# Kernel optimization log

Measured on AMD Instinct MI355X. Metric: run time of the kernel, lower is better.

The kernel has to match this reference:

```python
import jax, jax.numpy as jnp
import numpy as np

N = 120000   # nodes
E = 1200000  # edges
F_IN = 14    # PascalVOC-SP node features
H = 64       # args.hidden
C = 21       # num_classes
EPS = 1e-5


def _glorot(k, shape):
    fan_in = shape[0]
    return jax.random.normal(k, shape, jnp.float32) / np.sqrt(fan_in).astype(np.float32)


def setup_inputs() -> dict:
    key = jax.random.key(0)
    ks = jax.random.split(key, 16)
    inp = {}
    inp['x1'] = jax.random.normal(ks[0], (N, F_IN), jnp.float32)
    inp['edge_index'] = jax.random.randint(ks[1], (2, E), 0, N)
    dims = [(F_IN, H), (H, H), (H, H), (H, H)]
    i = 2
    for l, (din, dout) in enumerate(dims, 1):
        inp[f'Wn{l}'] = _glorot(ks[i], (din, dout)); i += 1
        inp[f'Wr{l}'] = _glorot(ks[i], (din, dout)); i += 1
        inp[f'b{l}'] = jnp.zeros((dout,), jnp.float32)
    for l in (1, 2, 3):
        inp[f'g{l}'] = jnp.ones((H,), jnp.float32)
        inp[f'be{l}'] = jnp.zeros((H,), jnp.float32)
    inp['Wm0'] = _glorot(ks[10], (H, H))
    inp['gm0'] = jnp.ones((H,), jnp.float32)
    inp['bem0'] = jnp.zeros((H,), jnp.float32)
    inp['Wm1'] = _glorot(ks[11], (H, H))
    inp['gm1'] = jnp.ones((H,), jnp.float32)
    inp['bem1'] = jnp.zeros((H,), jnp.float32)
    inp['Wm2'] = _glorot(ks[12], (H, C))
    inp['bm2'] = jnp.zeros((C,), jnp.float32)
    return inp


def _bn(x, g, b):
    # BatchNorm1d forward with batch statistics (train-mode normalization, biased var)
    m = x.mean(axis=0)
    v = x.var(axis=0)
    return (x - m) * jax.lax.rsqrt(v + EPS) * g + b


def _sage(x, src, dst, Wn, Wr, b):
    # PyG SAGEConv (mean aggr): out = mean_neighbors @ Wn + b + x @ Wr
    s = jax.ops.segment_sum(x[src], dst, num_segments=N)        # [N, d]
    cnt = jax.ops.segment_sum(jnp.ones((src.shape[0],), x.dtype), dst, num_segments=N)
    mean = s / jnp.maximum(cnt, 1.0)[:, None]
    return mean @ Wn + b + x @ Wr


def _lrelu(z):
    return jnp.where(z > 0, z, 0.01 * z)


def reference(x1, edge_index, Wn1, Wr1, b1, Wn2, Wr2, b2, Wn3, Wr3, b3, Wn4, Wr4, b4,
              g1, be1, g2, be2, g3, be3, Wm0, gm0, bem0, Wm1, gm1, bem1, Wm2, bm2):
    src, dst = edge_index[0], edge_index[1]
    x = _bn(_lrelu(_sage(x1, src, dst, Wn1, Wr1, b1)), g1, be1)   # conv1 + bano1 (dropout off)
    x = _bn(_lrelu(_sage(x, src, dst, Wn2, Wr2, b2)), g2, be2)    # conv2 + bano2
    x = _bn(jax.nn.relu(_sage(x, src, dst, Wn3, Wr3, b3)), g3, be3)  # conv3 + bano3
    x = _sage(x, src, dst, Wn4, Wr4, b4)                          # conv4
    # mlpRep: Linear(no bias)->BN->ReLU x2, then Linear(bias), no final act
    x = jax.nn.relu(_bn(x @ Wm0, gm0, bem0))
    x = jax.nn.relu(_bn(x @ Wm1, gm1, bem1))
    return x @ Wm2 + bm2
```

## Files before the change

kernel.cpp:

```cpp
#include <hip/hip_runtime.h>

constexpr int NN = 120000;
constexpr int EE = 1200000;
constexpr float EPSV = 1e-5f;
constexpr int NCBLK   = (NN + 127) / 128;
constexpr int NMFMABLK = NN / 64;
constexpr int ASTRIDE = 32;
constexpr int NSLOT = 64;

constexpr int BNODES  = 128;
constexpr int NBUCK   = (NN + BNODES - 1) / BNODES;
constexpr int BSTRIDE = 1536;
constexpr int EPB3    = 4096;
constexpr int NB3     = (EE + EPB3 - 1) / EPB3;
constexpr int NSTATF  = 5*NSLOT*128;

typedef __attribute__((ext_vector_type(8))) short bf8v;
typedef __attribute__((ext_vector_type(4))) float f4v;

__device__ __forceinline__ float bf2f(unsigned short u){
  union { unsigned i; float f; } v; v.i = ((unsigned)u) << 16; return v.f;
}
__device__ __forceinline__ unsigned short f2bf(float f){
  union { float f; unsigned i; } v; v.f = f;
  unsigned u = v.i;
  return (unsigned short)((u + 0x7FFFu + ((u >> 16) & 1u)) >> 16);
}
__device__ __forceinline__ unsigned pack2(float a, float b){
  return (unsigned)f2bf(a) | ((unsigned)f2bf(b) << 16);
}
__device__ __forceinline__ float act_f(float z, int ACT){
  if (ACT == 1) return z > 0.0f ? z : 0.01f*z;
  if (ACT == 2) return fmaxf(z, 0.0f);
  return z;
}
__device__ __forceinline__ void acc8(uint4 u, float& a0, float& a1, float& a2, float& a3,
                                     float& a4, float& a5, float& a6, float& a7){
  a0 += bf2f((unsigned short)(u.x & 0xFFFF)); a1 += bf2f((unsigned short)(u.x >> 16));
  a2 += bf2f((unsigned short)(u.y & 0xFFFF)); a3 += bf2f((unsigned short)(u.y >> 16));
  a4 += bf2f((unsigned short)(u.z & 0xFFFF)); a5 += bf2f((unsigned short)(u.z >> 16));
  a6 += bf2f((unsigned short)(u.w & 0xFFFF)); a7 += bf2f((unsigned short)(u.w >> 16));
}

__global__ __launch_bounds__(512) void k_bucket(const int* __restrict__ src, const int* __restrict__ dst,
                                                int* __restrict__ cursor, unsigned* __restrict__ bucketed,
                                                float* __restrict__ stats,
                                                const float* __restrict__ x, unsigned* __restrict__ xb){
  __shared__ int hist[NBUCK];
  __shared__ int lstart[NBUCK];
  const int tid = threadIdx.x;
  const int e0  = blockIdx.x * EPB3;
  for (int i = blockIdx.x*512 + tid; i < NSTATF; i += NB3*512) stats[i] = 0.0f;
  for (int i = blockIdx.x*512 + tid; i < NN*8; i += NB3*512){
    int n = i >> 3, j = i & 7;
    int c0 = 2*j, c1 = 2*j + 1;
    float f0 = (c0 < 14) ? x[(size_t)n*14 + c0] : 0.0f;
    float f1 = (c1 < 14) ? x[(size_t)n*14 + c1] : 0.0f;
    xb[i] = pack2(f0, f1);
  }
  for (int i = tid; i < NBUCK; i += 512) hist[i] = 0;
  __syncthreads();

  const bool full = (e0 + EPB3 <= EE);
  if (full){
    #pragma unroll 4
    for (int k = 0; k < EPB3/512; k++){
      int d = dst[e0 + k*512 + tid];
      atomicAdd(&hist[d >> 7], 1);
    }
  } else {
    #pragma unroll 1
    for (int k = 0; k < EPB3/512; k++){
      int e = e0 + k*512 + tid;
      if (e < EE){
        int d = dst[e];
        atomicAdd(&hist[d >> 7], 1);
      }
    }
  }
  __syncthreads();
  for (int i = tid; i < NBUCK; i += 512){
    int h = hist[i];
    lstart[i] = (h > 0) ? atomicAdd(&cursor[i], h) : 0;
  }
  __syncthreads();
  for (int i = tid; i < NBUCK; i += 512) hist[i] = 0;
  __syncthreads();
  #pragma unroll 1
  for (int k = 0; k < EPB3/512; k++){
    int e = e0 + k*512 + tid;
    if (e < EE){
      int d = dst[e];
      int s = src[e];
      int b = d >> 7;
      int r = atomicAdd(&hist[b], 1);
      int idx = lstart[b] + r;
      if (idx < BSTRIDE)
        bucketed[(size_t)b*BSTRIDE + idx] = ((unsigned)s << 7) | (unsigned)(d & 127);
    }
  }
}

__global__ __launch_bounds__(256) void k_buildadj(const unsigned* __restrict__ bucketed,
                                                  const int* __restrict__ cursor,
                                                  int* __restrict__ cnt, int* __restrict__ adj,
                                                  float* __restrict__ invdeg){
  __shared__ alignas(16) int ladj[BNODES*ASTRIDE];
  __shared__ int lcnt[BNODES];
  const int tid = threadIdx.x;
  const int b   = blockIdx.x;
  if (tid < BNODES) lcnt[tid] = 0;
  __syncthreads();
  const int tot = min(cursor[b], BSTRIDE);
  const unsigned* rp = bucketed + (size_t)b*BSTRIDE;
  for (int e = tid; e < tot; e += 256){
    unsigned rec = rp[e];
    int d = (int)(rec & 127u);
    int s = (int)(rec >> 7);
    int p = atomicAdd(&lcnt[d], 1);
    if (p < ASTRIDE) ladj[d*ASTRIDE + p] = s;
  }
  __syncthreads();
  int4* ap = (int4*)(adj + (size_t)b*BNODES*ASTRIDE);
  const int4* lp = (const int4*)ladj;
  #pragma unroll
  for (int i = 0; i < (BNODES*ASTRIDE/4)/256; i++)
    ap[i*256 + tid] = lp[i*256 + tid];
  if (tid < BNODES){
    int c = lcnt[tid];
    int n = b*BNODES + tid;
    cnt[n] = c;
    invdeg[n] = (c > 0) ? (1.0f/(float)c) : -1.0f;
  }
}

__global__ __launch_bounds__(256) void k_prep_conv_frag(const float* __restrict__ Wn, const float* __restrict__ Wr,
                                                        const float* __restrict__ b, const float* __restrict__ statSlots,
                                                        const float* __restrict__ g, const float* __restrict__ be,
                                                        unsigned short* __restrict__ frag, float* __restrict__ bias2){
  __shared__ float sc[64], sh[64];
  int t = threadIdx.x;
  if (t < 64){
    float sum = 0.0f, sq = 0.0f;
    #pragma unroll 8
    for (int s = 0; s < NSLOT; s++){
      sum += statSlots[s*128 + t];
      sq  += statSlots[s*128 + 64 + t];
    }
    float m = sum * (1.0f/NN);
    float v = sq * (1.0f/NN) - m*m;
    float a = g[t] * rsqrtf(v + EPSV);
    sc[t] = a; sh[t] = be[t] - m*a;
  }
  __syncthreads();
  if (blockIdx.x == 0 && t < 64){
    float accB = b[t], accN = 0.0f;
    for (int k=0;k<64;k++){
      accB += sh[k]*Wr[k*64+t];
      accN += sh[k]*Wn[k*64+t];
    }
    bias2[t]      = accB;
    bias2[64 + t] = accN;
  }
  {
    int idx = blockIdx.x*256 + t;
    int j    = idx & 7;
    int lane = (idx >> 3) & 63;
    int kk   = (idx >> 9) & 1;
    int ct   = (idx >> 10) & 3;
    int mat  = (idx >> 12) & 1;
    int k    = kk*32 + (lane >> 4)*8 + j;
    int col  = ct*16 + (lane & 15);
    const float* W = mat ? Wr : Wn;
    frag[idx] = f2bf(sc[k] * W[k*64 + col]);
  }
}

__global__ __launch_bounds__(256) void k_prep_lin_frag(const float* __restrict__ W,
                                                       unsigned short* __restrict__ frag,
                                                       float* __restrict__ bias2,
                                                       const float* __restrict__ bnSlots,
                                                       float* __restrict__ bnRed){
  int t = threadIdx.x;
  if (blockIdx.x == 0 && t < 128){
    bias2[t] = 0.0f;
    if (bnSlots){
      float s = 0.0f;
      #pragma unroll 8
      for (int sl = 0; sl < NSLOT; sl++) s += bnSlots[sl*128 + t];
      bnRed[t] = s;
    }
  }
  {
    int idx = blockIdx.x*256 + t;
    int j    = idx & 7;
    int lane = (idx >> 3) & 63;
    int kk   = (idx >> 9) & 1;
    int ct   = (idx >> 10) & 3;
    int k    = kk*32 + (lane >> 4)*8 + j;
    int col  = ct*16 + (lane & 15);
    frag[idx] = f2bf(W[k*64 + col]);
  }
}

__global__ __launch_bounds__(64) void k_prep_aff(const float* __restrict__ st,
                                                 const float* __restrict__ g, const float* __restrict__ be,
                                                 float* __restrict__ aff){
  int t = threadIdx.x;
  float s = 0.0f, q = 0.0f;
  #pragma unroll 8
  for (int sl = 0; sl < NSLOT; sl++){
    s += st[sl*128 + t];
    q += st[sl*128 + 64 + t];
  }
  float m = s*(1.0f/NN);
  float v = q*(1.0f/NN) - m*m;
  float a = g[t]*rsqrtf(v+EPSV);
  aff[t]      = a;
  aff[64 + t] = be[t] - m*a;
}

template<int ACT, bool STATS>
__global__ __launch_bounds__(256, 1) void k_gmfma(const unsigned short* __restrict__ X,
                                                  const int* __restrict__ cnt, const int* __restrict__ adj,
                                                  const float* __restrict__ invdeg,
                                                  const unsigned short* __restrict__ frag,
                                                  const float* __restrict__ bias2,
                                                  unsigned short* __restrict__ out,
                                                  float* __restrict__ statsOut){
  __shared__ unsigned short sMean[64*72];
  __shared__ float sst[512];
  const int tid  = threadIdx.x;
  const int lane = tid & 63;
  const int wv   = tid >> 6;
  const int nb0  = blockIdx.x*64;

  {
    const int q8 = lane & 7;
    const int h8 = lane >> 3;
    #pragma unroll
    for (int t8 = 0; t8 < 2; t8++){
      const int row = wv*16 + h8*2 + t8;
      const int n   = nb0 + row;
      const int d   = min(cnt[n], ASTRIDE);
      const int st  = n*ASTRIDE;
      float a0=0,a1=0,a2=0,a3=0,a4=0,a5=0,a6=0,a7=0;
      int j = 0;
      for (; j + 7 < d; j += 8){
        int4 sa = *(const int4*)(adj + st + j);
        int4 sb = *(const int4*)(adj + st + j + 4);
        uint4 u0 = *(const uint4*)(X + (size_t)sa.x*64 + 8*q8);
        uint4 u1 = *(const uint4*)(X + (size_t)sa.y*64 + 8*q8);
        uint4 u2 = *(const uint4*)(X + (size_t)sa.z*64 + 8*q8);
        uint4 u3 = *(const uint4*)(X + (size_t)sa.w*64 + 8*q8);
        uint4 u4 = *(const uint4*)(X + (size_t)sb.x*64 + 8*q8);
        uint4 u5 = *(const uint4*)(X + (size_t)sb.y*64 + 8*q8);
        uint4 u6 = *(const uint4*)(X + (size_t)sb.z*64 + 8*q8);
        uint4 u7 = *(const uint4*)(X + (size_t)sb.w*64 + 8*q8);
        acc8(u0,a0,a1,a2,a3,a4,a5,a6,a7); acc8(u1,a0,a1,a2,a3,a4,a5,a6,a7);
        acc8(u2,a0,a1,a2,a3,a4,a5,a6,a7); acc8(u3,a0,a1,a2,a3,a4,a5,a6,a7);
        acc8(u4,a0,a1,a2,a3,a4,a5,a6,a7); acc8(u5,a0,a1,a2,a3,a4,a5,a6,a7);
        acc8(u6,a0,a1,a2,a3,a4,a5,a6,a7); acc8(u7,a0,a1,a2,a3,a4,a5,a6,a7);
      }
      for (; j + 3 < d; j += 4){
        int4 sa = *(const int4*)(adj + st + j);
        uint4 u0 = *(const uint4*)(X + (size_t)sa.x*64 + 8*q8);
        uint4 u1 = *(const uint4*)(X + (size_t)sa.y*64 + 8*q8);
        uint4 u2 = *(const uint4*)(X + (size_t)sa.z*64 + 8*q8);
        uint4 u3 = *(const uint4*)(X + (size_t)sa.w*64 + 8*q8);
        acc8(u0,a0,a1,a2,a3,a4,a5,a6,a7); acc8(u1,a0,a1,a2,a3,a4,a5,a6,a7);
        acc8(u2,a0,a1,a2,a3,a4,a5,a6,a7); acc8(u3,a0,a1,a2,a3,a4,a5,a6,a7);
      }
      for (; j < d; j++){
        int s = adj[st + j];
        uint4 u = *(const uint4*)(X + (size_t)s*64 + 8*q8);
        acc8(u,a0,a1,a2,a3,a4,a5,a6,a7);
      }
      float iv = fmaxf(invdeg[n], 0.0f);
      uint4 o;
      o.x = pack2(a0*iv, a1*iv);
      o.y = pack2(a2*iv, a3*iv);
      o.z = pack2(a4*iv, a5*iv);
      o.w = pack2(a6*iv, a7*iv);
      *(uint4*)(sMean + row*72 + 8*q8) = o;
    }
  }

  const bf8v* fp = (const bf8v*)frag;
  bf8v wn[4][2], wr[4][2];
  #pragma unroll
  for (int ct=0;ct<4;ct++){
    #pragma unroll
    for (int kk=0;kk<2;kk++){
      wn[ct][kk] = fp[((0*4+ct)*2+kk)*64 + lane];
      wr[ct][kk] = fp[((1*4+ct)*2+kk)*64 + lane];
    }
  }
  const int m  = lane & 15;
  const int kq = lane >> 4;
  const size_t arow = (size_t)(nb0 + wv*16 + m)*64;
  bf8v ax0 = *(const bf8v*)(X + arow + kq*8);
  bf8v ax1 = *(const bf8v*)(X + arow + 32 + kq*8);
  __syncthreads();
  bf8v am0 = *(const bf8v*)(sMean + (wv*16 + m)*72 + kq*8);
  bf8v am1 = *(const bf8v*)(sMean + (wv*16 + m)*72 + 32 + kq*8);

  f4v acc[4];
  #pragma unroll
  for (int ct=0;ct<4;ct++){
    f4v c = {0.0f,0.0f,0.0f,0.0f};
    c = __builtin_amdgcn_mfma_f32_16x16x32_bf16(am0, wn[ct][0], c, 0,0,0);
    c = __builtin_amdgcn_mfma_f32_16x16x32_bf16(am1, wn[ct][1], c, 0,0,0);
    c = __builtin_amdgcn_mfma_f32_16x16x32_bf16(ax0, wr[ct][0], c, 0,0,0);
    c = __builtin_amdgcn_mfma_f32_16x16x32_bf16(ax1, wr[ct][1], c, 0,0,0);
    acc[ct] = c;
  }

  const int col = lane & 15;
  float bb[4], bg[4];
  #pragma unroll
  for (int ct=0;ct<4;ct++){
    bb[ct] = bias2[ct*16 + col];
    bg[ct] = bias2[64 + ct*16 + col];
  }
  float ls[4] = {0,0,0,0}, lq[4] = {0,0,0,0};
  #pragma unroll
  for (int r=0;r<4;r++){
    const int node = nb0 + wv*16 + (lane>>4)*4 + r;
    float gadd = (invdeg[node] > 0.0f) ? 1.0f : 0.0f;
    #pragma unroll
    for (int ct=0;ct<4;ct++){
      float z = acc[ct][r] + bb[ct] + gadd * bg[ct];
      z = act_f(z, ACT);
      out[(size_t)node*64 + ct*16 + col] = f2bf(z);
      if (STATS){ ls[ct] += z; lq[ct] = fmaf(z, z, lq[ct]); }
    }
  }
  if constexpr (STATS){
    #pragma unroll
    for (int ct=0;ct<4;ct++){
      float s = ls[ct]; s += __shfl_down(s, 32); s += __shfl_down(s, 16);
      float q = lq[ct]; q += __shfl_down(q, 32); q += __shfl_down(q, 16);
      if (kq == 0){
        sst[wv*128 + ct*16 + col]      = s;
        sst[wv*128 + 64 + ct*16 + col] = q;
      }
    }
    __syncthreads();
    if (tid < 128){
      float v = sst[tid] + sst[128+tid] + sst[256+tid] + sst[384+tid];
      atomicAdd(&statsOut[(blockIdx.x & (NSLOT-1))*128 + tid], v);
    }
  }
}

template<int ACT, bool STATS, bool BNA>
__global__ __launch_bounds__(256, 1) void k_mfma_lin(const unsigned short* __restrict__ Ax,
                                                     const unsigned short* __restrict__ frag,
                                                     const float* __restrict__ bias2,
                                                     unsigned short* __restrict__ out,
                                                     float* __restrict__ statsOut,
                                                     const float* __restrict__ bnRed,
                                                     const float* __restrict__ bnG,
                                                     const float* __restrict__ bnB){
  __shared__ float sst[512];
  const int lane = threadIdx.x & 63;
  const int wv   = threadIdx.x >> 6;
  const int n0   = (blockIdx.x*4 + wv)*16;
  const int m    = lane & 15;
  const int kq   = lane >> 4;

  const bf8v* fp = (const bf8v*)frag;
  bf8v wr[4][2];
  #pragma unroll
  for (int ct=0;ct<4;ct++){
    #pragma unroll
    for (int kk=0;kk<2;kk++) wr[ct][kk] = fp[(ct*2+kk)*64 + lane];
  }

  const size_t arow = (size_t)(n0 + m)*64;
  bf8v ax0 = *(const bf8v*)(Ax + arow + kq*8);
  bf8v ax1 = *(const bf8v*)(Ax + arow + 32 + kq*8);
  if constexpr (BNA){
    #pragma unroll
    for (int j=0;j<8;j++){
      int k0 = kq*8 + j, k1 = 32 + kq*8 + j;
      float m0 = bnRed[k0]*(1.0f/NN);
      float v0 = bnRed[64+k0]*(1.0f/NN) - m0*m0;
      float a0 = bnG[k0]*rsqrtf(v0+EPSV);
      float b0 = bnB[k0] - m0*a0;
      ax0[j] = (short)f2bf(fmaxf(fmaf(a0, bf2f((unsigned short)ax0[j]), b0), 0.0f));
      float m1 = bnRed[k1]*(1.0f/NN);
      float v1 = bnRed[64+k1]*(1.0f/NN) - m1*m1;
      float a1 = bnG[k1]*rsqrtf(v1+EPSV);
      float b1 = bnB[k1] - m1*a1;
      ax1[j] = (short)f2bf(fmaxf(fmaf(a1, bf2f((unsigned short)ax1[j]), b1), 0.0f));
    }
  }

  f4v acc[4];
  #pragma unroll
  for (int ct=0;ct<4;ct++){
    f4v c = {0.0f,0.0f,0.0f,0.0f};
    c = __builtin_amdgcn_mfma_f32_16x16x32_bf16(ax0, wr[ct][0], c, 0,0,0);
    c = __builtin_amdgcn_mfma_f32_16x16x32_bf16(ax1, wr[ct][1], c, 0,0,0);
    acc[ct] = c;
  }

  const int col = lane & 15;
  float bb[4];
  #pragma unroll
  for (int ct=0;ct<4;ct++) bb[ct] = bias2[ct*16 + col];
  float ls[4] = {0,0,0,0}, lq[4] = {0,0,0,0};
  #pragma unroll
  for (int r=0;r<4;r++){
    const int node = n0 + (lane>>4)*4 + r;
    #pragma unroll
    for (int ct=0;ct<4;ct++){
      float z = act_f(acc[ct][r] + bb[ct], ACT);
      out[(size_t)node*64 + ct*16 + col] = f2bf(z);
      if (STATS){ ls[ct] += z; lq[ct] = fmaf(z, z, lq[ct]); }
    }
  }
  if constexpr (STATS){
    #pragma unroll
    for (int ct=0;ct<4;ct++){
      float s = ls[ct]; s += __shfl_down(s, 32); s += __shfl_down(s, 16);
      float q = lq[ct]; q += __shfl_down(q, 32); q += __shfl_down(q, 16);
      if (kq == 0){
        sst[wv*128 + ct*16 + col]      = s;
        sst[wv*128 + 64 + ct*16 + col] = q;
      }
    }
    __syncthreads();
    if (threadIdx.x < 128){
      float v = sst[threadIdx.x] + sst[128+threadIdx.x] + sst[256+threadIdx.x] + sst[384+threadIdx.x];
      atomicAdd(&statsOut[(blockIdx.x & (NSLOT-1))*128 + threadIdx.x], v);
    }
  }
}

__global__ __launch_bounds__(512, 1) void k_conv1(const unsigned* __restrict__ xb, const float* __restrict__ x,
                                                  const int* __restrict__ cnt, const int* __restrict__ adj,
                                                  const float* __restrict__ invdeg,
                                                  const float* __restrict__ Wn, const float* __restrict__ Wr,
                                                  const float* __restrict__ b,
                                                  unsigned short* __restrict__ out, float* __restrict__ statsOut){
  constexpr int DIN = 14, RS = 15;
  __shared__ float sMean[128*RS];
  __shared__ float sX[128*RS];
  __shared__ float sst[8*128];
  const int tid  = threadIdx.x;
  const int lane = tid & 63;
  const int wv   = tid >> 6;
  const int p    = tid & 3;
  const int nl   = tid >> 2;
  const int n0   = blockIdx.x*128;
  const int n    = n0 + nl;
  const bool valid = (n < NN);
  const int c0   = p*16;

  {
    const float* gp = x + (size_t)n0*DIN;
    for (int i = tid; i < 128*DIN; i += 512){
      int r = i / DIN, c = i - r*DIN;
      sX[r*RS + c] = (n0 + r < NN) ? gp[i] : 0.0f;
    }
  }

  {
    float mm[14];
    #pragma unroll
    for (int j=0;j<14;j++) mm[j] = 0.0f;
    const int d  = valid ? min(cnt[n], ASTRIDE) : 0;
    const int st = n*ASTRIDE;
    for (int j=p; j<d; j+=4){
      int s = adj[st+j];
      const uint4* rp = (const uint4*)(xb + s*8);
      uint4 u0 = rp[0], u1 = rp[1];
      mm[0]+=bf2f((unsigned short)(u0.x&0xFFFF)); mm[1]+=bf2f((unsigned short)(u0.x>>16));
      mm[2]+=bf2f((unsigned short)(u0.y&0xFFFF)); mm[3]+=bf2f((unsigned short)(u0.y>>16));
      mm[4]+=bf2f((unsigned short)(u0.z&0xFFFF)); mm[5]+=bf2f((unsigned short)(u0.z>>16));
      mm[6]+=bf2f((unsigned short)(u0.w&0xFFFF)); mm[7]+=bf2f((unsigned short)(u0.w>>16));
      mm[8]+=bf2f((unsigned short)(u1.x&0xFFFF)); mm[9]+=bf2f((unsigned short)(u1.x>>16));
      mm[10]+=bf2f((unsigned short)(u1.y&0xFFFF)); mm[11]+=bf2f((unsigned short)(u1.y>>16));
      mm[12]+=bf2f((unsigned short)(u1.z&0xFFFF)); mm[13]+=bf2f((unsigned short)(u1.z>>16));
    }
    #pragma unroll
    for (int j=0;j<14;j++){
      mm[j] += __shfl_xor(mm[j], 1);
      mm[j] += __shfl_xor(mm[j], 2);
    }
    float iv = valid ? invdeg[n] : -1.0f;
    float gate = (iv > 0.0f) ? iv : 0.0f;
    if (p == 0){
      #pragma unroll
      for (int j=0;j<14;j++) sMean[nl*RS + j] = mm[j]*gate;
    }
  }
  __syncthreads();

  float acc[16];
  #pragma unroll
  for (int jj=0;jj<16;jj++) acc[jj] = 0.0f;
  #pragma unroll 1
  for (int k=0;k<DIN;k++){
    float rv = sMean[nl*RS + k];
    const float* wr = Wn + k*64 + c0;
    #pragma unroll
    for (int jj=0;jj<16;jj++) acc[jj] = fmaf(wr[jj], rv, acc[jj]);
  }
  #pragma unroll 1
  for (int k=0;k<DIN;k++){
    float rv = sX[nl*RS + k];
    const float* wr = Wr + k*64 + c0;
    #pragma unroll
    for (int jj=0;jj<16;jj++) acc[jj] = fmaf(wr[jj], rv, acc[jj]);
  }

  float vs[16], vq[16];
  #pragma unroll
  for (int q=0;q<16;q++){
    float z = valid ? act_f(acc[q] + b[c0+q], 1) : 0.0f;
    vs[q] = z; vq[q] = z*z;
  }
  if (valid){
    uint4 t0, t1;
    t0.x = pack2(vs[0],vs[1]);   t0.y = pack2(vs[2],vs[3]);
    t0.z = pack2(vs[4],vs[5]);   t0.w = pack2(vs[6],vs[7]);
    t1.x = pack2(vs[8],vs[9]);   t1.y = pack2(vs[10],vs[11]);
    t1.z = pack2(vs[12],vs[13]); t1.w = pack2(vs[14],vs[15]);
    uint4* op = (uint4*)(out + (size_t)n*64 + c0);
    op[0] = t0; op[1] = t1;
  }

  #pragma unroll
  for (int k=0;k<4;k++){
    const bool keep1 = ((lane >> (k+2)) & 1) != 0;
    const int half = 16 >> (k+1);
    #pragma unroll
    for (int i=0;i<half;i++){
      float sa = vs[2*i], sb = vs[2*i+1];
      float qa = vq[2*i], qb = vq[2*i+1];
      float skeep = keep1 ? sb : sa;
      float ssend = keep1 ? sa : sb;
      float qkeep = keep1 ? qb : qa;
      float qsend = keep1 ? qa : qb;
      vs[i] = skeep + __shfl_xor(ssend, 4<<k);
      vq[i] = qkeep + __shfl_xor(qsend, 4<<k);
    }
  }
  const int f = c0 + (lane>>2);
  sst[wv*128 + f]      = vs[0];
  sst[wv*128 + 64 + f] = vq[0];
  __syncthreads();
  if (tid < 128){
    float v = 0.0f;
    #pragma unroll
    for (int w=0;w<8;w++) v += sst[w*128 + tid];
    atomicAdd(&statsOut[(blockIdx.x & (NSLOT-1))*128 + tid], v);
  }
}

__global__ __launch_bounds__(256, 1) void k_lin21(const unsigned short* __restrict__ x,
                                                  const float* __restrict__ W, const float* __restrict__ bias,
                                                  const float* __restrict__ aff,
                                                  float* __restrict__ out){
  __shared__ float sW[64*21];
  __shared__ float sAff[128];
  const int tid = threadIdx.x;
  if (tid < 128) sAff[tid] = aff[tid];
  for (int i = tid; i < 64*21; i += 256) sW[i] = W[i];
  __syncthreads();

  const int p  = tid & 3;
  const int nl = tid >> 2;
  const int n  = blockIdx.x*64 + nl;
  const bool valid = (n < NN);
  const int k0 = p*16;

  uint4 u0 = {0,0,0,0}, u1 = {0,0,0,0};
  if (valid){
    const unsigned short* rp = x + (size_t)n*64 + k0;
    u0 = *(const uint4*)(rp);
    u1 = *(const uint4*)(rp + 8);
  }
  float f[16];
  f[0]=bf2f((unsigned short)(u0.x&0xFFFF)); f[1]=bf2f((unsigned short)(u0.x>>16));
  f[2]=bf2f((unsigned short)(u0.y&0xFFFF)); f[3]=bf2f((unsigned short)(u0.y>>16));
  f[4]=bf2f((unsigned short)(u0.z&0xFFFF)); f[5]=bf2f((unsigned short)(u0.z>>16));
  f[6]=bf2f((unsigned short)(u0.w&0xFFFF)); f[7]=bf2f((unsigned short)(u0.w>>16));
  f[8]=bf2f((unsigned short)(u1.x&0xFFFF)); f[9]=bf2f((unsigned short)(u1.x>>16));
  f[10]=bf2f((unsigned short)(u1.y&0xFFFF)); f[11]=bf2f((unsigned short)(u1.y>>16));
  f[12]=bf2f((unsigned short)(u1.z&0xFFFF)); f[13]=bf2f((unsigned short)(u1.z>>16));
  f[14]=bf2f((unsigned short)(u1.w&0xFFFF)); f[15]=bf2f((unsigned short)(u1.w>>16));
  #pragma unroll
  for (int j=0;j<16;j++)
    f[j] = fmaxf(fmaf(sAff[k0+j], f[j], sAff[64+k0+j]), 0.0f);

  float a[21];
  #pragma unroll
  for (int jj=0;jj<21;jj++) a[jj] = 0.0f;
  #pragma unroll
  for (int k=0;k<16;k++){
    const float* wr = sW + (k0+k)*21;
    float rv = f[k];
    #pragma unroll
    for (int jj=0;jj<21;jj++) a[jj] = fmaf(wr[jj], rv, a[jj]);
  }
  #pragma unroll
  for (int jj=0;jj<21;jj++){
    a[jj] += __shfl_xor(a[jj], 1);
    a[jj] += __shfl_xor(a[jj], 2);
  }
  if (valid){
    const int c0 = p*6;
    const int ce = (p == 3) ? 21 : c0 + 6;
    float* op = out + (size_t)n*21;
    #pragma unroll 6
    for (int jj=c0; jj<ce; jj++) op[jj] = a[jj] + bias[jj];
  }
}

extern "C" void kernel_launch(void* const* d_in, const int* in_sizes, int n_in,
                              void* d_out, int out_size, void* d_ws, size_t ws_size,
                              hipStream_t stream){
  const float* x1  = (const float*)d_in[0];
  const int*   ei  = (const int*)d_in[1];
  const int* srcp = ei;
  const int* dstp = ei + EE;
  const float *Wn1=(const float*)d_in[2],  *Wr1=(const float*)d_in[3],  *b1=(const float*)d_in[4];
  const float *Wn2=(const float*)d_in[5],  *Wr2=(const float*)d_in[6],  *b2=(const float*)d_in[7];
  const float *Wn3=(const float*)d_in[8],  *Wr3=(const float*)d_in[9],  *b3=(const float*)d_in[10];
  const float *Wn4=(const float*)d_in[11], *Wr4=(const float*)d_in[12], *b4=(const float*)d_in[13];
  const float *g1=(const float*)d_in[14], *be1=(const float*)d_in[15];
  const float *g2=(const float*)d_in[16], *be2=(const float*)d_in[17];
  const float *g3=(const float*)d_in[18], *be3=(const float*)d_in[19];
  const float *Wm0=(const float*)d_in[20], *gm0=(const float*)d_in[21], *bem0=(const float*)d_in[22];
  const float *Wm1=(const float*)d_in[23], *gm1=(const float*)d_in[24], *bem1=(const float*)d_in[25];
  const float *Wm2=(const float*)d_in[26], *bm2=(const float*)d_in[27];
  float* out = (float*)d_out;

  char* ws = (char*)d_ws;
  int*   cnt     = (int*)(ws);
  float* invdeg  = (float*)(ws + (1ull<<20));
  int*   adj     = (int*)(ws + (2ull<<20));
  unsigned short* hA   = (unsigned short*)(ws + (25ull<<20));
  unsigned short* hB   = (unsigned short*)(ws + (41ull<<20));
  float* stats   = (float*)(ws + (57ull<<20));
  float* bnRed   = (float*)(ws + (57ull<<20) + 192*1024);
  float* aff5    = (float*)(ws + (57ull<<20) + 224*1024);
  unsigned short* fragC = (unsigned short*)(ws + (58ull<<20));
  float* bias2C  = (float*)(ws + (58ull<<20) + 65536);
  unsigned short* fragL = (unsigned short*)(ws + (59ull<<20));
  float* bias2L  = (float*)(ws + (59ull<<20) + 65536);
  unsigned* xb   = (unsigned*)(ws + (60ull<<20));
  unsigned* bucketed = (unsigned*)(ws + (25ull<<20));
  int* cursor        = (int*)(ws + (25ull<<20) + (6ull<<20));

  float* S1 = stats;
  float* S2 = stats + NSLOT*128;
  float* S3 = stats + 2*NSLOT*128;
  float* S4 = stats + 3*NSLOT*128;
  float* S5 = stats + 4*NSLOT*128;

  hipMemsetAsync(cursor, 0, NBUCK*sizeof(int), stream);
  k_bucket  <<<NB3,  512,0,stream>>>(srcp, dstp, cursor, bucketed, stats, x1, xb);
  k_buildadj<<<NBUCK,256,0,stream>>>(bucketed, cursor, cnt, adj, invdeg);

  k_conv1<<<NCBLK,512,0,stream>>>(xb,x1,cnt,adj,invdeg,Wn1,Wr1,b1,hA,S1);

  k_prep_conv_frag<<<32,256,0,stream>>>(Wn2,Wr2,b2,S1,g1,be1,fragC,bias2C);
  k_gmfma<1,true><<<NMFMABLK,256,0,stream>>>(hA,cnt,adj,invdeg,fragC,bias2C,hB,S2);

  k_prep_conv_frag<<<32,256,0,stream>>>(Wn3,Wr3,b3,S2,g2,be2,fragC,bias2C);
  k_gmfma<2,true><<<NMFMABLK,256,0,stream>>>(hB,cnt,adj,invdeg,fragC,bias2C,hA,S3);

  k_prep_conv_frag<<<32,256,0,stream>>>(Wn4,Wr4,b4,S3,g3,be3,fragC,bias2C);
  k_gmfma<0,false><<<NMFMABLK,256,0,stream>>>(hA,cnt,adj,invdeg,fragC,bias2C,hB,nullptr);

  k_prep_lin_frag<<<16,256,0,stream>>>(Wm0, fragL, bias2L, nullptr, nullptr);
  k_mfma_lin<0,true,false><<<NMFMABLK,256,0,stream>>>(hB,fragL,bias2L,hA,S4,nullptr,nullptr,nullptr);

  k_prep_lin_frag<<<16,256,0,stream>>>(Wm1, fragL, bias2L, S4, bnRed);
  k_mfma_lin<0,true,true><<<NMFMABLK,256,0,stream>>>(hA,fragL,bias2L,hB,S5,bnRed,gm0,bem0);

  k_prep_aff<<<1,64,0,stream>>>(S5, gm1, bem1, aff5);
  k_lin21<<<NMFMABLK,256,0,stream>>>(hB,Wm2,bm2,aff5,out);
}
```

Before: 397.6 us.

## Rewrite conv1 as MFMA kernel with concatenated mean/self bf16 fragments

Replaces the scalar-FMA first SAGE layer with an MFMA kernel. The mean-aggregated neighbour features and the bf16 self features are concatenated into one K=32 operand, and a new prep kernel builds the matching Wn/Wr weight fragment. The gather is restructured so lanes load half-rows of the bf16 feature table, and the dense projection becomes a single 16x16x32 bf16 MFMA per column tile. The self features now come from the bf16 copy rather than fp32 x, which lowers precision, and one extra small kernel launch is added.

```diff
diff --git a/kernel.cpp b/kernel.cpp
--- a/kernel.cpp
+++ b/kernel.cpp
@@ -3,7 +3,6 @@
 constexpr int NN = 120000;
 constexpr int EE = 1200000;
 constexpr float EPSV = 1e-5f;
-constexpr int NCBLK   = (NN + 127) / 128;
 constexpr int NMFMABLK = NN / 64;
 constexpr int ASTRIDE = 32;
 constexpr int NSLOT = 64;
@@ -201,6 +200,23 @@
     int col  = ct*16 + (lane & 15);
     frag[idx] = f2bf(W[k*64 + col]);
   }
+}
+
+__global__ __launch_bounds__(256) void k_prep_c1_frag(const float* __restrict__ Wn, const float* __restrict__ Wr,
+                                                      const float* __restrict__ b,
+                                                      unsigned short* __restrict__ frag, float* __restrict__ bias2){
+  int t = threadIdx.x;
+  int idx = blockIdx.x*256 + t;
+  int j    = idx & 7;
+  int lane = (idx >> 3) & 63;
+  int ct   = (idx >> 9) & 3;
+  int k    = (lane >> 4)*8 + j;
+  int col  = ct*16 + (lane & 15);
+  float w = 0.0f;
+  if (k < 14)                 w = Wn[k*64 + col];
+  else if (k >= 16 && k < 30) w = Wr[(k-16)*64 + col];
+  frag[idx] = f2bf(w);
+  if (blockIdx.x == 0 && t < 64) bias2[t] = b[t];
 }
 
 __global__ __launch_bounds__(64) void k_prep_aff(const float* __restrict__ st,
@@ -440,124 +456,109 @@
   }
 }
 
-__global__ __launch_bounds__(512, 1) void k_conv1(const unsigned* __restrict__ xb, const float* __restrict__ x,
-                                                  const int* __restrict__ cnt, const int* __restrict__ adj,
-                                                  const float* __restrict__ invdeg,
-                                                  const float* __restrict__ Wn, const float* __restrict__ Wr,
-                                                  const float* __restrict__ b,
-                                                  unsigned short* __restrict__ out, float* __restrict__ statsOut){
-  constexpr int DIN = 14, RS = 15;
-  __shared__ float sMean[128*RS];
-  __shared__ float sX[128*RS];
-  __shared__ float sst[8*128];
+__global__ __launch_bounds__(256, 1) void k_conv1m(const unsigned* __restrict__ xb,
+                                                   const int* __restrict__ cnt, const int* __restrict__ adj,
+                                                   const float* __restrict__ invdeg,
+                                                   const unsigned short* __restrict__ frag,
+                                                   const float* __restrict__ bias2,
+                                                   unsigned short* __restrict__ out,
+                                                   float* __restrict__ statsOut){
+  __shared__ unsigned short sMean[64*24];
+  __shared__ float sst[512];
   const int tid  = threadIdx.x;
   const int lane = tid & 63;
   const int wv   = tid >> 6;
-  const int p    = tid & 3;
-  const int nl   = tid >> 2;
-  const int n0   = blockIdx.x*128;
-  const int n    = n0 + nl;
-  const bool valid = (n < NN);
-  const int c0   = p*16;
+  const int nb0  = blockIdx.x*64;
 
   {
-    const float* gp = x + (size_t)n0*DIN;
-    for (int i = tid; i < 128*DIN; i += 512){
-      int r = i / DIN, c = i - r*DIN;
-      sX[r*RS + c] = (n0 + r < NN) ? gp[i] : 0.0f;
-    }
-  }
-
-  {
-    float mm[14];
-    #pragma unroll
-    for (int j=0;j<14;j++) mm[j] = 0.0f;
-    const int d  = valid ? min(cnt[n], ASTRIDE) : 0;
-    const int st = n*ASTRIDE;
-    for (int j=p; j<d; j+=4){
-      int s = adj[st+j];
-      const uint4* rp = (const uint4*)(xb + s*8);
-      uint4 u0 = rp[0], u1 = rp[1];
-      mm[0]+=bf2f((unsigned short)(u0.x&0xFFFF)); mm[1]+=bf2f((unsigned short)(u0.x>>16));
-      mm[2]+=bf2f((unsigned short)(u0.y&0xFFFF)); mm[3]+=bf2f((unsigned short)(u0.y>>16));
-      mm[4]+=bf2f((unsigned short)(u0.z&0xFFFF)); mm[5]+=bf2f((unsigned short)(u0.z>>16));
-      mm[6]+=bf2f((unsigned short)(u0.w&0xFFFF)); mm[7]+=bf2f((unsigned short)(u0.w>>16));
-      mm[8]+=bf2f((unsigned short)(u1.x&0xFFFF)); mm[9]+=bf2f((unsigned short)(u1.x>>16));
-      mm[10]+=bf2f((unsigned short)(u1.y&0xFFFF)); mm[11]+=bf2f((unsigned short)(u1.y>>16));
-      mm[12]+=bf2f((unsigned short)(u1.z&0xFFFF)); mm[13]+=bf2f((unsigned short)(u1.z>>16));
-    }
-    #pragma unroll
-    for (int j=0;j<14;j++){
-      mm[j] += __shfl_xor(mm[j], 1);
-      mm[j] += __shfl_xor(mm[j], 2);
-    }
-    float iv = valid ? invdeg[n] : -1.0f;
-    float gate = (iv > 0.0f) ? iv : 0.0f;
-    if (p == 0){
-      #pragma unroll
-      for (int j=0;j<14;j++) sMean[nl*RS + j] = mm[j]*gate;
-    }
-  }
-  __syncthreads();
-
-  float acc[16];
-  #pragma unroll
-  for (int jj=0;jj<16;jj++) acc[jj] = 0.0f;
-  #pragma unroll 1
-  for (int k=0;k<DIN;k++){
-    float rv = sMean[nl*RS + k];
-    const float* wr = Wn + k*64 + c0;
-    #pragma unroll
-    for (int jj=0;jj<16;jj++) acc[jj] = fmaf(wr[jj], rv, acc[jj]);
-  }
-  #pragma unroll 1
-  for (int k=0;k<DIN;k++){
-    float rv = sX[nl*RS + k];
-    const float* wr = Wr + k*64 + c0;
-    #pragma unroll
-    for (int jj=0;jj<16;jj++) acc[jj] = fmaf(wr[jj], rv, acc[jj]);
-  }
-
-  float vs[16], vq[16];
-  #pragma unroll
-  for (int q=0;q<16;q++){
-    float z = valid ? act_f(acc[q] + b[c0+q], 1) : 0.0f;
-    vs[q] = z; vq[q] = z*z;
-  }
-  if (valid){
-    uint4 t0, t1;
-    t0.x = pack2(vs[0],vs[1]);   t0.y = pack2(vs[2],vs[3]);
-    t0.z = pack2(vs[4],vs[5]);   t0.w = pack2(vs[6],vs[7]);
-    t1.x = pack2(vs[8],vs[9]);   t1.y = pack2(vs[10],vs[11]);
-    t1.z = pack2(vs[12],vs[13]); t1.w = pack2(vs[14],vs[15]);
-    uint4* op = (uint4*)(out + (size_t)n*64 + c0);
-    op[0] = t0; op[1] = t1;
-  }
-
-  #pragma unroll
-  for (int k=0;k<4;k++){
-    const bool keep1 = ((lane >> (k+2)) & 1) != 0;
-    const int half = 16 >> (k+1);
-    #pragma unroll
-    for (int i=0;i<half;i++){
-      float sa = vs[2*i], sb = vs[2*i+1];
-      float qa = vq[2*i], qb = vq[2*i+1];
-      float skeep = keep1 ? sb : sa;
-      float ssend = keep1 ? sa : sb;
-      float qkeep = keep1 ? qb : qa;
-      float qsend = keep1 ? qa : qb;
-      vs[i] = skeep + __shfl_xor(ssend, 4<<k);
-      vq[i] = qkeep + __shfl_xor(qsend, 4<<k);
-    }
-  }
-  const int f = c0 + (lane>>2);
-  sst[wv*128 + f]      = vs[0];
-  sst[wv*128 + 64 + f] = vq[0];
+    const int q2 = lane & 1;
+    const int g  = (lane >> 1) & 1;
+    const int nd = lane >> 2;
+    const int row = wv*16 + nd;
+    const int n   = nb0 + row;
+    const int d   = min(cnt[n], ASTRIDE);
+    const int st  = n*ASTRIDE;
+    float a0=0,a1=0,a2=0,a3=0,a4=0,a5=0,a6=0,a7=0;
+    int j = g;
+    for (; j + 2 < d; j += 4){
+      int s0 = adj[st + j];
+      int s1 = adj[st + j + 2];
+      uint4 u0 = *(const uint4*)(xb + s0*8 + q2*4);
+      uint4 u1 = *(const uint4*)(xb + s1*8 + q2*4);
+      acc8(u0,a0,a1,a2,a3,a4,a5,a6,a7);
+      acc8(u1,a0,a1,a2,a3,a4,a5,a6,a7);
+    }
+    if (j < d){
+      int s0 = adj[st + j];
+      uint4 u0 = *(const uint4*)(xb + s0*8 + q2*4);
+      acc8(u0,a0,a1,a2,a3,a4,a5,a6,a7);
+    }
+    a0 += __shfl_xor(a0, 2); a1 += __shfl_xor(a1, 2);
+    a2 += __shfl_xor(a2, 2); a3 += __shfl_xor(a3, 2);
+    a4 += __shfl_xor(a4, 2); a5 += __shfl_xor(a5, 2);
+    a6 += __shfl_xor(a6, 2); a7 += __shfl_xor(a7, 2);
+    if (g == 0){
+      float iv = fmaxf(invdeg[n], 0.0f);
+      uint4 o;
+      o.x = pack2(a0*iv, a1*iv);
+      o.y = pack2(a2*iv, a3*iv);
+      o.z = pack2(a4*iv, a5*iv);
+      o.w = pack2(a6*iv, a7*iv);
+      *(uint4*)(sMean + row*24 + q2*8) = o;
+    }
+  }
+
+  const bf8v* fp = (const bf8v*)frag;
+  bf8v wb[4];
+  #pragma unroll
+  for (int ct=0;ct<4;ct++) wb[ct] = fp[ct*64 + lane];
+
+  const int m  = lane & 15;
+  const int kq = lane >> 4;
+  __syncthreads();
+  bf8v av;
+  if (kq < 2){
+    av = *(const bf8v*)(sMean + (wv*16 + m)*24 + kq*8);
+  } else {
+    const unsigned short* xr = (const unsigned short*)xb + (size_t)(nb0 + wv*16 + m)*16;
+    av = *(const bf8v*)(xr + (kq-2)*8);
+  }
+
+  f4v acc[4];
+  #pragma unroll
+  for (int ct=0;ct<4;ct++){
+    f4v c = {0.0f,0.0f,0.0f,0.0f};
+    c = __builtin_amdgcn_mfma_f32_16x16x32_bf16(av, wb[ct], c, 0,0,0);
+    acc[ct] = c;
+  }
+
+  const int col = lane & 15;
+  float bb[4];
+  #pragma unroll
+  for (int ct=0;ct<4;ct++) bb[ct] = bias2[ct*16 + col];
+  float ls[4] = {0,0,0,0}, lq[4] = {0,0,0,0};
+  #pragma unroll
+  for (int r=0;r<4;r++){
+    const int node = nb0 + wv*16 + (lane>>4)*4 + r;
+    #pragma unroll
+    for (int ct=0;ct<4;ct++){
+      float z = act_f(acc[ct][r] + bb[ct], 1);
+      out[(size_t)node*64 + ct*16 + col] = f2bf(z);
+      ls[ct] += z; lq[ct] = fmaf(z, z, lq[ct]);
+    }
+  }
+  #pragma unroll
+  for (int ct=0;ct<4;ct++){
+    float s = ls[ct]; s += __shfl_down(s, 32); s += __shfl_down(s, 16);
+    float q = lq[ct]; q += __shfl_down(q, 32); q += __shfl_down(q, 16);
+    if (kq == 0){
+      sst[wv*128 + ct*16 + col]      = s;
+      sst[wv*128 + 64 + ct*16 + col] = q;
+    }
+  }
   __syncthreads();
   if (tid < 128){
-    float v = 0.0f;
-    #pragma unroll
-    for (int w=0;w<8;w++) v += sst[w*128 + tid];
+    float v = sst[tid] + sst[128+tid] + sst[256+tid] + sst[384+tid];
     atomicAdd(&statsOut[(blockIdx.x & (NSLOT-1))*128 + tid], v);
   }
 }
@@ -655,6 +656,8 @@
   unsigned short* fragL = (unsigned short*)(ws + (59ull<<20));
   float* bias2L  = (float*)(ws + (59ull<<20) + 65536);
   unsigned* xb   = (unsigned*)(ws + (60ull<<20));
+  unsigned short* frag1 = (unsigned short*)(ws + (64ull<<20));
+  float* bias1   = (float*)(ws + (64ull<<20) + 8192);
   unsigned* bucketed = (unsigned*)(ws + (25ull<<20));
   int* cursor        = (int*)(ws + (25ull<<20) + (6ull<<20));
 
@@ -668,7 +671,8 @@
   k_bucket  <<<NB3,  512,0,stream>>>(srcp, dstp, cursor, bucketed, stats, x1, xb);
   k_buildadj<<<NBUCK,256,0,stream>>>(bucketed, cursor, cnt, adj, invdeg);
 
-  k_conv1<<<NCBLK,512,0,stream>>>(xb,x1,cnt,adj,invdeg,Wn1,Wr1,b1,hA,S1);
+  k_prep_c1_frag<<<8,256,0,stream>>>(Wn1, Wr1, b1, frag1, bias1);
+  k_conv1m<<<NMFMABLK,256,0,stream>>>(xb, cnt, adj, invdeg, frag1, bias1, hA, S1);
 
   k_prep_conv_frag<<<32,256,0,stream>>>(Wn2,Wr2,b2,S1,g1,be1,fragC,bias2C);
   k_gmfma<1,true><<<NMFMABLK,256,0,stream>>>(hA,cnt,adj,invdeg,fragC,bias2C,hB,S2);
```

After: 348.6 us. -12.3%, faster.
